# Kernel optimization log

Hardware: AMD Instinct MI355X
Metric: run time of the kernel (lower is better)

The kernel has to match this reference:

```python
import jax, jax.numpy as jnp
import numpy as np

N = 20000      # nodes
E = 100000     # edges
B = 128        # graphs in batch
F_IN = 14      # node feature dim
DIM = 64       # hidden dim
E_FEAT = 4     # edge feature dim
MLP_H = 128    # edge MLP hidden


def setup_inputs() -> dict:
    key = jax.random.key(0)
    ks = jax.random.split(key, 26)

    def rn(k, shape, fan_in):
        return jax.random.normal(k, shape, jnp.float32) / np.sqrt(fan_in)

    d = {}
    d['x'] = jax.random.normal(ks[0], (N, F_IN), jnp.float32)
    d['edge_attr'] = jax.random.uniform(ks[1], (E, E_FEAT), jnp.float32)
    d['edge_index'] = jax.random.randint(ks[2], (2, E), 0, N)
    d['batch'] = jnp.sort(jax.random.randint(ks[3], (N,), 0, B))
    # lin0
    d['lin0_w'] = rn(ks[4], (F_IN, DIM), F_IN)
    d['lin0_b'] = jnp.zeros((DIM,), jnp.float32)
    # edge MLP: Linear(4,128) -> ReLU -> Linear(128, dim*dim)
    d['mlp_w1'] = rn(ks[5], (E_FEAT, MLP_H), E_FEAT)
    d['mlp_b1'] = jnp.zeros((MLP_H,), jnp.float32)
    d['mlp_w2'] = rn(ks[6], (MLP_H, DIM * DIM), MLP_H) * 0.1
    d['mlp_b2'] = jnp.zeros((DIM * DIM,), jnp.float32)
    # NNConv root weight + bias
    d['conv_root'] = rn(ks[7], (DIM, DIM), DIM)
    d['conv_bias'] = jnp.zeros((DIM,), jnp.float32)
    # GRU (input dim DIM, hidden DIM), torch gate order r,z,n
    d['gru_wi'] = rn(ks[8], (DIM, 3 * DIM), DIM)
    d['gru_wh'] = rn(ks[9], (DIM, 3 * DIM), DIM)
    d['gru_bi'] = jnp.zeros((3 * DIM,), jnp.float32)
    d['gru_bh'] = jnp.zeros((3 * DIM,), jnp.float32)
    # Set2Set LSTM (input 2*DIM, hidden DIM), torch gate order i,f,g,o
    d['lstm_wi'] = rn(ks[10], (2 * DIM, 4 * DIM), 2 * DIM)
    d['lstm_wh'] = rn(ks[11], (DIM, 4 * DIM), DIM)
    d['lstm_bi'] = jnp.zeros((4 * DIM,), jnp.float32)
    d['lstm_bh'] = jnp.zeros((4 * DIM,), jnp.float32)
    # output head
    d['lin1_w'] = rn(ks[12], (2 * DIM, DIM), 2 * DIM)
    d['lin1_b'] = jnp.zeros((DIM,), jnp.float32)
    d['lin2_w'] = rn(ks[13], (DIM, 1), DIM)
    d['lin2_b'] = jnp.zeros((1,), jnp.float32)
    return d


def _forward(x, edge_attr, edge_index, batch,
             lin0_w, lin0_b, mlp_w1, mlp_b1, mlp_w2, mlp_b2,
             conv_root, conv_bias,
             gru_wi, gru_wh, gru_bi, gru_bh,
             lstm_wi, lstm_wh, lstm_bi, lstm_bh,
             lin1_w, lin1_b, lin2_w, lin2_b):
    src, dst = edge_index[0], edge_index[1]

    out = jax.nn.relu(x @ lin0_w + lin0_b)            # [N, DIM]
    h = out                                            # GRU hidden

    # per-edge weight matrices from edge MLP (shared across the 3 steps)
    ew = jax.nn.relu(edge_attr @ mlp_w1 + mlp_b1) @ mlp_w2 + mlp_b2
    ew = ew.reshape(E, DIM, DIM)                       # [E, DIM, DIM]
    # incoming-edge counts for scatter-mean
    cnt = jax.ops.segment_sum(jnp.ones((E,), jnp.float32), dst, num_segments=N)
    cnt = jnp.maximum(cnt, 1.0)[:, None]

    for _ in range(3):
        msg = jnp.einsum('ei,eio->eo', out[src], ew)   # gather + per-edge matmul
        agg = jax.ops.segment_sum(msg, dst, num_segments=N) / cnt
        m = jax.nn.relu(agg + out @ conv_root + conv_bias)
        # GRU cell (torch gate order: r, z, n)
        gi = m @ gru_wi + gru_bi
        gh = h @ gru_wh + gru_bh
        r = jax.nn.sigmoid(gi[:, :DIM] + gh[:, :DIM])
        z = jax.nn.sigmoid(gi[:, DIM:2 * DIM] + gh[:, DIM:2 * DIM])
        n = jnp.tanh(gi[:, 2 * DIM:] + r * gh[:, 2 * DIM:])
        h = (1.0 - z) * n + z * h
        out = h

    # Set2Set pooling, 3 processing steps
    q_star = jnp.zeros((B, 2 * DIM), jnp.float32)
    hl = jnp.zeros((B, DIM), jnp.float32)
    cl = jnp.zeros((B, DIM), jnp.float32)
    for _ in range(3):
        gates = q_star @ lstm_wi + hl @ lstm_wh + lstm_bi + lstm_bh  # [B, 4*DIM]
        i = jax.nn.sigmoid(gates[:, :DIM])
        f = jax.nn.sigmoid(gates[:, DIM:2 * DIM])
        g = jnp.tanh(gates[:, 2 * DIM:3 * DIM])
        o = jax.nn.sigmoid(gates[:, 3 * DIM:])
        cl = f * cl + i * g
        hl = o * jnp.tanh(cl)
        q = hl                                         # [B, DIM]
        e = jnp.sum(out * q[batch], axis=-1)           # [N]
        emax = jax.ops.segment_max(e, batch, num_segments=B)
        emax = jnp.where(jnp.isfinite(emax), emax, 0.0)
        a = jnp.exp(e - emax[batch])
        asum = jax.ops.segment_sum(a, batch, num_segments=B)
        a = a / jnp.maximum(asum, 1e-16)[batch]
        r_vec = jax.ops.segment_sum(a[:, None] * out, batch, num_segments=B)
        q_star = jnp.concatenate([q, r_vec], axis=-1)  # [B, 2*DIM]

    y = jax.nn.relu(q_star @ lin1_w + lin1_b) @ lin2_w + lin2_b
    return y.reshape(-1)                               # [B]


def reference(x, edge_attr, edge_index, batch,
              lin0_w, lin0_b, mlp_w1, mlp_b1, mlp_w2, mlp_b2,
              conv_root, conv_bias,
              gru_wi, gru_wh, gru_bi, gru_bh,
              lstm_wi, lstm_wh, lstm_bi, lstm_bh,
              lin1_w, lin1_b, lin2_w, lin2_b):
    return _forward(x, edge_attr, edge_index, batch,
                    lin0_w, lin0_b, mlp_w1, mlp_b1, mlp_w2, mlp_b2,
                    conv_root, conv_bias,
                    gru_wi, gru_wh, gru_bi, gru_bh,
                    lstm_wi, lstm_wh, lstm_bi, lstm_bh,
                    lin1_w, lin1_b, lin2_w, lin2_b)
```

## Files before the change

kernel.cpp:

```cpp
#include <hip/hip_runtime.h>
#include <math.h>

#define N_ 20000
#define E_ 100000
#define B_ 128
#define F_IN_ 14
#define DIM_ 64
#define E_FEAT_ 4
#define MLP_H_ 128
#define EWC_ 4096
#define PC_ 8192
#define PC2_ 8256

#define LIN0_BLKS 5000
#define DEG_BLKS 391
#define PREPB_BLKS 2064

typedef __attribute__((ext_vector_type(4))) float f32x4;
typedef __attribute__((ext_vector_type(8))) _Float16 halfx8;

__global__ __launch_bounds__(256) void setup_a(
        const float* __restrict__ x, const float* __restrict__ lw,
        const float* __restrict__ lb, float* __restrict__ out,
        const int* __restrict__ src, const int* __restrict__ dst,
        float* __restrict__ cnt, int* __restrict__ cnt_src,
        const int* __restrict__ batch, int* __restrict__ off_b,
        const float* __restrict__ w2, const float* __restrict__ b2,
        _Float16* __restrict__ Bf) {
    int b = blockIdx.x;
    int t = threadIdx.x;
    if (b < LIN0_BLKS) {
        int idx = b * 256 + t;
        int n = idx >> 6, d = idx & 63;
        float acc = lb[d];
#pragma unroll
        for (int f = 0; f < F_IN_; ++f) acc = fmaf(x[n * F_IN_ + f], lw[f * DIM_ + d], acc);
        out[idx] = acc > 0.f ? acc : 0.f;
    } else if (b < LIN0_BLKS + DEG_BLKS) {
        int e = (b - LIN0_BLKS) * 256 + t;
        if (e < E_) {
            atomicAdd(&cnt[dst[e]], 1.0f);
            atomicAdd(&cnt_src[src[e]], 1);
        }
        if (b == LIN0_BLKS && t <= B_) {
            int bb = t;
            int lo = 0, hi = N_;
            while (lo < hi) {
                int mid = (lo + hi) >> 1;
                if (batch[mid] < bb) lo = mid + 1; else hi = mid;
            }
            off_b[bb] = lo;
        }
    } else {
        int idx = (b - LIN0_BLKS - DEG_BLKS) * 256 + t;
        if (idx >= PC2_ * 64) return;
        int c16 = idx >> 10;
        int r   = idx & 1023;
        int ks  = r >> 9;
        int q   = (r >> 7) & 3;
        int lr  = (r >> 3) & 15;
        int j   = r & 7;
        int c = c16 * 16 + lr;
        int i = ks * 32 + q * 8 + j;
        float v;
        if (c < PC_) {
            int o = c >> 7, k = c & 127;
            v = w2[(size_t)k * EWC_ + i * 64 + o];
        } else {
            int o = c - PC_;
            v = b2[i * 64 + o];
        }
        Bf[idx] = (_Float16)v;
    }
}

__global__ void scan_src(const int* __restrict__ cnt_src, int* __restrict__ src_off) {
    __shared__ int part[256];
    __shared__ int off[257];
    int t = threadIdx.x;
    const int per = (N_ + 255) / 256;
    int base = t * per;
    int s = 0;
    for (int i = 0; i < per; ++i) { int b = base + i; if (b < N_) s += cnt_src[b]; }
    part[t] = s;
    __syncthreads();
    if (t == 0) {
        int a = 0;
        for (int i = 0; i < 256; ++i) { off[i] = a; a += part[i]; }
        off[256] = a;
    }
    __syncthreads();
    int run = off[t];
    for (int i = 0; i < per; ++i) {
        int b = base + i;
        if (b < N_) { src_off[b] = run; run += cnt_src[b]; }
    }
    if (t == 0) src_off[N_] = off[256];
}

__global__ __launch_bounds__(256) void scatter_mlp1(
        const int* __restrict__ src, const int* __restrict__ dst,
        int* __restrict__ cur, const int* __restrict__ src_off,
        const float* __restrict__ ea, const float* __restrict__ w1,
        const float* __restrict__ b1, int* __restrict__ dsts,
        _Float16* __restrict__ h1s) {
    __shared__ float w1s[E_FEAT_ * MLP_H_];
    __shared__ float b1s[MLP_H_];
    int t = threadIdx.x;
    if (t < MLP_H_) b1s[t] = b1[t];
    for (int i = t; i < E_FEAT_ * MLP_H_; i += 256) w1s[i] = w1[i];
    __syncthreads();
    int e = blockIdx.x * 256 + t;
    if (e >= E_) return;
    int s = src[e];
    int p = src_off[s] + atomicAdd(&cur[s], 1);
    dsts[p] = dst[e];
    float a0 = ea[e * 4 + 0], a1 = ea[e * 4 + 1];
    float a2 = ea[e * 4 + 2], a3 = ea[e * 4 + 3];
    _Float16* hrow = h1s + (size_t)p * 128;
#pragma unroll
    for (int k8 = 0; k8 < 16; ++k8) {
        halfx8 v;
#pragma unroll
        for (int j = 0; j < 8; ++j) {
            int k = k8 * 8 + j;
            float acc = b1s[k];
            acc = fmaf(a0, w1s[k], acc);
            acc = fmaf(a1, w1s[128 + k], acc);
            acc = fmaf(a2, w1s[256 + k], acc);
            acc = fmaf(a3, w1s[384 + k], acc);
            v[j] = (_Float16)(acc > 0.f ? acc : 0.f);
        }
        *(halfx8*)&hrow[k8 * 8] = v;
    }
}

__global__ __launch_bounds__(512, 4) void fused_msg(
        const float* __restrict__ out, const _Float16* __restrict__ Bf,
        const _Float16* __restrict__ h1s,
        const int* __restrict__ dsts, const int* __restrict__ src_off,
        float* __restrict__ agg) {
    __shared__ _Float16 Plds[16 * 2048];
    const int tid = threadIdx.x;
    const int lane = tid & 63;
    const int w = __builtin_amdgcn_readfirstlane(tid >> 6);
    const int lrow = lane & 15, quad = lane >> 4;
    const int nb0 = blockIdx.x * 16;

    halfx8 aG[2];
    {
        const float* orow = out + (size_t)(nb0 + lrow) * 64 + quad * 8;
#pragma unroll
        for (int ks = 0; ks < 2; ++ks) {
            float4 v0 = *(const float4*)(orow + ks * 32);
            float4 v1 = *(const float4*)(orow + ks * 32 + 4);
            aG[ks][0] = (_Float16)v0.x; aG[ks][1] = (_Float16)v0.y;
            aG[ks][2] = (_Float16)v0.z; aG[ks][3] = (_Float16)v0.w;
            aG[ks][4] = (_Float16)v1.x; aG[ks][5] = (_Float16)v1.y;
            aG[ks][6] = (_Float16)v1.z; aG[ks][7] = (_Float16)v1.w;
        }
    }

    f32x4 qf[4];
#pragma unroll
    for (int f = 0; f < 4; ++f) {
        const _Float16* bc = &Bf[(size_t)(512 + f) * 1024 + quad * 128 + lrow * 8];
        halfx8 bq0 = *(const halfx8*)bc;
        halfx8 bq1 = *(const halfx8*)(bc + 512);
        f32x4 z = (f32x4){0.f, 0.f, 0.f, 0.f};
        z = __builtin_amdgcn_mfma_f32_16x16x32_f16(aG[0], bq0, z, 0, 0, 0);
        z = __builtin_amdgcn_mfma_f32_16x16x32_f16(aG[1], bq1, z, 0, 0, 0);
        qf[f] = z;
    }

    const int n0g = nb0 + 2 * w;
    const int beg0 = src_off[n0g];
    const int end0 = src_off[n0g + 1];
    const int end1 = src_off[n0g + 2];

#pragma unroll
    for (int p = 0; p < 4; ++p) {
        if (p) __syncthreads();

#pragma unroll 8
        for (int nf = 0; nf < 16; ++nf) {
            int cl = w * 256 + nf * 16 + lrow;
            size_t tb = (size_t)(p * 128 + w * 16 + nf) * 1024 + quad * 128 + lrow * 8;
            halfx8 b0 = *(const halfx8*)&Bf[tb];
            halfx8 b1 = *(const halfx8*)&Bf[tb + 512];
            f32x4 acc = (f32x4){0.f, 0.f, 0.f, 0.f};
            acc = __builtin_amdgcn_mfma_f32_16x16x32_f16(aG[0], b0, acc, 0, 0, 0);
            acc = __builtin_amdgcn_mfma_f32_16x16x32_f16(aG[1], b1, acc, 0, 0, 0);
            int o = cl >> 7, k = cl & 127;
            int kz = k ^ (quad << 5) ^ ((o & 7) << 3);
            int base = o * 2048 + kz;
#pragma unroll
            for (int rr = 0; rr < 4; ++rr)
                Plds[base + (quad * 4 + rr) * 128] = (_Float16)acc[rr];
        }
        __syncthreads();

        int o0 = p * 16;
#pragma unroll
        for (int nn = 0; nn < 2; ++nn) {
            int nl = 2 * w + nn;
            int beg = nn ? end0 : beg0;
            int endv = nn ? end1 : end0;
            if (beg == endv) continue;
            int srcl = ((nl >> 2) << 4) | lrow;
            int rsel = nl & 3;
            float qel = rsel == 0 ? qf[p][0] : rsel == 1 ? qf[p][1]
                      : rsel == 2 ? qf[p][2] : qf[p][3];
            float qv = __shfl(qel, srcl, 64);
            halfx8 bf[4];
#pragma unroll
            for (int ks = 0; ks < 4; ++ks) {
                int kk = (ks * 32 + quad * 8) ^ ((nl >> 2) << 5) ^ ((lrow & 7) << 3);
                bf[ks] = *(const halfx8*)&Plds[lrow * 2048 + nl * 128 + kk];
            }
            for (int g = beg; g < endv; g += 16) {
                int gcnt = endv - g; if (gcnt > 16) gcnt = 16;
                int ei = lrow < gcnt ? lrow : gcnt - 1;
                int gi = g + ei;
                int dv = dsts[gi];
                halfx8 af[4];
#pragma unroll
                for (int ks = 0; ks < 4; ++ks)
                    af[ks] = *(const halfx8*)&h1s[(size_t)gi * 128 + ks * 32 + quad * 8];
                f32x4 acc = (f32x4){0.f, 0.f, 0.f, 0.f};
#pragma unroll
                for (int ks = 0; ks < 4; ++ks)
                    acc = __builtin_amdgcn_mfma_f32_16x16x32_f16(
                        af[ks], bf[ks], acc, 0, 0, 0);
#pragma unroll
                for (int rr = 0; rr < 4; ++rr) {
                    int j = quad * 4 + rr;
                    int d = __shfl(dv, j, 64);
                    if (j < gcnt) {
                        atomicAdd(&agg[(size_t)d * 64 + o0 + lrow], acc[rr] + qv);
                    }
                }
            }
        }
    }
}

__global__ __launch_bounds__(256) void gru_kernel(float* __restrict__ out,
                                                  float* __restrict__ agg,
                                                  const float* __restrict__ cnt,
                                                  const float* __restrict__ root,
                                                  const float* __restrict__ cbias,
                                                  const float* __restrict__ wi,
                                                  const float* __restrict__ wh,
                                                  const float* __restrict__ bi,
                                                  const float* __restrict__ bh) {
    __shared__ float root_s[64 * 64];
    __shared__ float h_s[64 * 64];
    __shared__ float m_s[64 * 64];
    int tid = threadIdx.x;
    int lane = tid & 63;
    int wv = __builtin_amdgcn_readfirstlane(tid >> 6);
    int nb = blockIdx.x * 64;
#pragma unroll
    for (int it = 0; it < 4; ++it) {
        int i = it * 1024 + tid * 4;
        *(float4*)&root_s[i] = *(const float4*)&root[i];
    }
#pragma unroll
    for (int it = 0; it < 4; ++it) {
        int i = it * 1024 + tid * 4;
        int gidx = nb * 64 + i;
        float4 v = gidx < N_ * 64 ? *(const float4*)&out[gidx]
                                  : (float4){0.f, 0.f, 0.f, 0.f};
        *(float4*)&h_s[i] = v;
    }
    __syncthreads();

    int nbase = nb + wv * 16;
    float a[16];
#pragma unroll
    for (int j = 0; j < 16; ++j) {
        int n = nbase + j;
        if (n < N_) {
            float c = cnt[n]; c = c > 1.f ? c : 1.f;
            a[j] = agg[(size_t)n * 64 + lane] / c + cbias[lane];
            agg[(size_t)n * 64 + lane] = 0.f;
        } else {
            a[j] = 0.f;
        }
    }
    for (int i = 0; i < 64; ++i) {
        float rv = root_s[i * 64 + lane];
#pragma unroll
        for (int j = 0; j < 16; ++j)
            a[j] = fmaf(h_s[(wv * 16 + j) * 64 + i], rv, a[j]);
    }
#pragma unroll
    for (int j = 0; j < 16; ++j)
        m_s[(wv * 16 + j) * 64 + lane] = a[j] > 0.f ? a[j] : 0.f;
    __syncthreads();

    float gr[16], gz[16], gn[16];
    {
        float b0 = bi[lane], b1 = bi[64 + lane], b2v = bi[128 + lane];
#pragma unroll
        for (int j = 0; j < 16; ++j) { gr[j] = b0; gz[j] = b1; gn[j] = b2v; }
    }
    for (int i = 0; i < 64; ++i) {
        float w0 = wi[i * 192 + lane];
        float w1 = wi[i * 192 + 64 + lane];
        float w2v = wi[i * 192 + 128 + lane];
#pragma unroll
        for (int j = 0; j < 16; ++j) {
            float mi = m_s[(wv * 16 + j) * 64 + i];
            gr[j] = fmaf(mi, w0, gr[j]);
            gz[j] = fmaf(mi, w1, gz[j]);
            gn[j] = fmaf(mi, w2v, gn[j]);
        }
    }
    float hr[16], hz[16], hn[16];
    {
        float b0 = bh[lane], b1 = bh[64 + lane], b2v = bh[128 + lane];
#pragma unroll
        for (int j = 0; j < 16; ++j) { hr[j] = b0; hz[j] = b1; hn[j] = b2v; }
    }
    for (int i = 0; i < 64; ++i) {
        float u0 = wh[i * 192 + lane];
        float u1 = wh[i * 192 + 64 + lane];
        float u2 = wh[i * 192 + 128 + lane];
#pragma unroll
        for (int j = 0; j < 16; ++j) {
            float hi = h_s[(wv * 16 + j) * 64 + i];
            hr[j] = fmaf(hi, u0, hr[j]);
            hz[j] = fmaf(hi, u1, hz[j]);
            hn[j] = fmaf(hi, u2, hn[j]);
        }
    }
#pragma unroll
    for (int j = 0; j < 16; ++j) {
        int n = nbase + j;
        if (n < N_) {
            float rg = 1.f / (1.f + expf(-(gr[j] + hr[j])));
            float zg = 1.f / (1.f + expf(-(gz[j] + hz[j])));
            float ng = tanhf(gn[j] + rg * hn[j]);
            float h = h_s[(wv * 16 + j) * 64 + lane];
            out[(size_t)n * 64 + lane] = (1.f - zg) * ng + zg * h;
        }
    }
}

__global__ __launch_bounds__(256) void lstm_all_kernel(
        const float* __restrict__ out, const int* __restrict__ off_b,
        float* __restrict__ e_ws,
        const float* __restrict__ wi, const float* __restrict__ wh,
        const float* __restrict__ bi, const float* __restrict__ bh,
        const float* __restrict__ hw1, const float* __restrict__ hb1,
        const float* __restrict__ hw2, const float* __restrict__ hb2,
        float* __restrict__ y) {
    int b = blockIdx.x;
    int t = threadIdx.x;
    __shared__ float qs[128], hs[64], cs[64], g[256];
    __shared__ float q[64];
    __shared__ float red[256], racc[256], sasum[4];

    if (t < 128) qs[t] = 0.f;
    if (t < 64) { hs[t] = 0.f; cs[t] = 0.f; }
    __syncthreads();

    int start = off_b[b], end = off_b[b + 1];

    for (int s = 0; s < 3; ++s) {
        {
            float acc = bi[t] + bh[t];
#pragma unroll 8
            for (int i = 0; i < 128; ++i) acc = fmaf(qs[i], wi[i * 256 + t], acc);
#pragma unroll 8
            for (int i = 0; i < 64; ++i) acc = fmaf(hs[i], wh[i * 256 + t], acc);
            g[t] = acc;
        }
        __syncthreads();
        if (t < 64) {
            float ig = 1.f / (1.f + expf(-g[t]));
            float fg = 1.f / (1.f + expf(-g[64 + t]));
            float gg = tanhf(g[128 + t]);
            float og = 1.f / (1.f + expf(-g[192 + t]));
            float c = fg * cs[t] + ig * gg;
            cs[t] = c;
            float h = og * tanhf(c);
            hs[t] = h;
            q[t] = h;
        }
        __syncthreads();

        float lmax = -1e30f;
        for (int n = start + t; n < end; n += 256) {
            float acc = 0.f;
#pragma unroll 16
            for (int d2 = 0; d2 < 64; ++d2) acc = fmaf(out[n * 64 + d2], q[d2], acc);
            e_ws[n] = acc;
            lmax = fmaxf(lmax, acc);
        }
        red[t] = lmax;
        __syncthreads();
        for (int s2 = 128; s2 > 0; s2 >>= 1) {
            if (t < s2) red[t] = fmaxf(red[t], red[t + s2]);
            __syncthreads();
        }
        float emax = red[0];
        int w = t >> 6, d = t & 63;
        float rl = 0.f, lasum = 0.f;
        for (int n = start + w; n < end; n += 4) {
            float a = expf(e_ws[n] - emax);
            rl = fmaf(a, out[n * 64 + d], rl);
            if (d == 0) lasum += a;
        }
        racc[t] = rl;
        if (d == 0) sasum[w] = lasum;
        __syncthreads();
        if (t < 64) {
            float r = racc[t] + racc[64 + t] + racc[128 + t] + racc[192 + t];
            float as = sasum[0] + sasum[1] + sasum[2] + sasum[3];
            as = fmaxf(as, 1e-16f);
            qs[t] = q[t];
            qs[64 + t] = r / as;
        }
        __syncthreads();
    }

    if (t < 64) {
        float acc = hb1[t];
#pragma unroll 8
        for (int i = 0; i < 128; ++i) acc = fmaf(qs[i], hw1[i * 64 + t], acc);
        acc = acc > 0.f ? acc : 0.f;
        float p = acc * hw2[t];
        for (int off = 32; off > 0; off >>= 1) p += __shfl_down(p, off, 64);
        if (t == 0) y[b] = p + hb2[0];
    }
}

extern "C" void kernel_launch(void* const* d_in, const int* in_sizes, int n_in,
                              void* d_out, int out_size, void* d_ws, size_t ws_size,
                              hipStream_t stream) {
    (void)in_sizes; (void)n_in; (void)out_size; (void)ws_size;
    const float* x        = (const float*)d_in[0];
    const float* ea       = (const float*)d_in[1];
    const int*   eidx     = (const int*)d_in[2];
    const int*   batch    = (const int*)d_in[3];
    const float* lin0_w   = (const float*)d_in[4];
    const float* lin0_b   = (const float*)d_in[5];
    const float* mlp_w1   = (const float*)d_in[6];
    const float* mlp_b1   = (const float*)d_in[7];
    const float* mlp_w2   = (const float*)d_in[8];
    const float* mlp_b2   = (const float*)d_in[9];
    const float* conv_root= (const float*)d_in[10];
    const float* conv_bias= (const float*)d_in[11];
    const float* gru_wi   = (const float*)d_in[12];
    const float* gru_wh   = (const float*)d_in[13];
    const float* gru_bi   = (const float*)d_in[14];
    const float* gru_bh   = (const float*)d_in[15];
    const float* lstm_wi  = (const float*)d_in[16];
    const float* lstm_wh  = (const float*)d_in[17];
    const float* lstm_bi  = (const float*)d_in[18];
    const float* lstm_bh  = (const float*)d_in[19];
    const float* lin1_w   = (const float*)d_in[20];
    const float* lin1_b   = (const float*)d_in[21];
    const float* lin2_w   = (const float*)d_in[22];
    const float* lin2_b   = (const float*)d_in[23];
    float* y = (float*)d_out;

    const int* src = eidx;
    const int* dst = eidx + E_;

    char* w = (char*)d_ws;
    auto carve = [&](size_t bytes) {
        char* p = w;
        w += (bytes + 255) & ~(size_t)255;
        return p;
    };
    float* out_buf = (float*)carve((size_t)N_ * DIM_ * 4);
    float* e_ws    = (float*)carve((size_t)N_ * 4);
    int*   off_b   = (int*)carve((size_t)(B_ + 1) * 4);
    _Float16* h1s  = (_Float16*)carve((size_t)E_ * MLP_H_ * 2);
    _Float16* Bf   = (_Float16*)carve((size_t)PC2_ * 64 * 2);
    int*   src_off = (int*)carve((size_t)(N_ + 1) * 4);
    int*   dsts    = (int*)carve((size_t)E_ * 4);
    char*  zero0   = w;
    float* agg     = (float*)carve((size_t)N_ * DIM_ * 4);
    float* cnt     = (float*)carve((size_t)N_ * 4);
    int*   cnt_src = (int*)carve((size_t)N_ * 4);
    int*   cur     = (int*)carve((size_t)N_ * 4);
    size_t zbytes  = (size_t)(w - zero0);

    hipMemsetAsync(zero0, 0, zbytes, stream);

    setup_a<<<LIN0_BLKS + DEG_BLKS + PREPB_BLKS, 256, 0, stream>>>(
        x, lin0_w, lin0_b, out_buf, src, dst, cnt, cnt_src, batch, off_b,
        mlp_w2, mlp_b2, Bf);
    scan_src<<<1, 256, 0, stream>>>(cnt_src, src_off);
    scatter_mlp1<<<(E_ + 255) / 256, 256, 0, stream>>>(src, dst, cur, src_off,
                                                       ea, mlp_w1, mlp_b1,
                                                       dsts, h1s);

    for (int step = 0; step < 3; ++step) {
        fused_msg<<<N_ / 16, 512, 0, stream>>>(out_buf, Bf, h1s, dsts,
                                               src_off, agg);
        gru_kernel<<<(N_ + 63) / 64, 256, 0, stream>>>(out_buf, agg, cnt,
                                                       conv_root, conv_bias,
                                                       gru_wi, gru_wh,
                                                       gru_bi, gru_bh);
    }

    lstm_all_kernel<<<B_, 256, 0, stream>>>(out_buf, off_b, e_ws,
                                            lstm_wi, lstm_wh, lstm_bi, lstm_bh,
                                            lin1_w, lin1_b, lin2_w, lin2_b, y);
}
```

Before: 614.3 us.

## Fuse message, GRU and Set2Set stages into one persistent kernel with grid barriers

Replaces the seven separate launches (three fused_msg/gru_kernel pairs plus the LSTM readout) with one persistent kernel of 512 blocks. Blocks grid-stride over node tiles and meet at atomic-counter barriers between stages, which removes launch gaps and tail effects between stages. The GRU stage now works on 32-node tiles and computes its input and hidden gate products in a single loop. The readout uses 512 threads per graph. The barrier depends on all 512 blocks being resident at once, which is assumed rather than guaranteed, and the smaller grid may expose less parallelism in the message stage.

Measured after the change: 2.007 ms. 3.27x slower.

```diff
diff --git a/kernel.cpp b/kernel.cpp
--- a/kernel.cpp
+++ b/kernel.cpp
@@ -15,6 +15,8 @@
 #define LIN0_BLKS 5000
 #define DEG_BLKS 391
 #define PREPB_BLKS 2064
+
+#define NBLK_ 512
 
 typedef __attribute__((ext_vector_type(4))) float f32x4;
 typedef __attribute__((ext_vector_type(8))) _Float16 halfx8;
@@ -135,306 +137,308 @@
     }
 }
 
-__global__ __launch_bounds__(512, 4) void fused_msg(
-        const float* __restrict__ out, const _Float16* __restrict__ Bf,
-        const _Float16* __restrict__ h1s,
-        const int* __restrict__ dsts, const int* __restrict__ src_off,
-        float* __restrict__ agg) {
-    __shared__ _Float16 Plds[16 * 2048];
+__device__ inline void gsync(int* cnt, int target) {
+    __syncthreads();
+    if (threadIdx.x == 0) {
+        __threadfence();
+        __hip_atomic_fetch_add(cnt, 1, __ATOMIC_ACQ_REL, __HIP_MEMORY_SCOPE_AGENT);
+        while (__hip_atomic_load(cnt, __ATOMIC_ACQUIRE, __HIP_MEMORY_SCOPE_AGENT) < target) {
+            __builtin_amdgcn_s_sleep(1);
+        }
+    }
+    __syncthreads();
+}
+
+__global__ __launch_bounds__(512, 4) void mega(
+        float* __restrict__ out, const _Float16* __restrict__ Bf,
+        const _Float16* __restrict__ h1s, const int* __restrict__ dsts,
+        const int* __restrict__ src_off, float* __restrict__ agg,
+        const float* __restrict__ cntf, const float* __restrict__ root,
+        const float* __restrict__ cbias, const float* __restrict__ gwi,
+        const float* __restrict__ gwh, const float* __restrict__ gbi,
+        const float* __restrict__ gbh, const int* __restrict__ off_b,
+        float* __restrict__ e_ws, const float* __restrict__ lwi,
+        const float* __restrict__ lwh, const float* __restrict__ lbi,
+        const float* __restrict__ lbh, const float* __restrict__ hw1,
+        const float* __restrict__ hb1, const float* __restrict__ hw2,
+        const float* __restrict__ hb2, float* __restrict__ y,
+        int* __restrict__ gcnt) {
+    __shared__ float smem_f[16384];
+    _Float16* Plds = (_Float16*)smem_f;
     const int tid = threadIdx.x;
     const int lane = tid & 63;
-    const int w = __builtin_amdgcn_readfirstlane(tid >> 6);
+    const int wv8 = __builtin_amdgcn_readfirstlane(tid >> 6);
     const int lrow = lane & 15, quad = lane >> 4;
-    const int nb0 = blockIdx.x * 16;
-
-    halfx8 aG[2];
-    {
-        const float* orow = out + (size_t)(nb0 + lrow) * 64 + quad * 8;
-#pragma unroll
-        for (int ks = 0; ks < 2; ++ks) {
-            float4 v0 = *(const float4*)(orow + ks * 32);
-            float4 v1 = *(const float4*)(orow + ks * 32 + 4);
-            aG[ks][0] = (_Float16)v0.x; aG[ks][1] = (_Float16)v0.y;
-            aG[ks][2] = (_Float16)v0.z; aG[ks][3] = (_Float16)v0.w;
-            aG[ks][4] = (_Float16)v1.x; aG[ks][5] = (_Float16)v1.y;
-            aG[ks][6] = (_Float16)v1.z; aG[ks][7] = (_Float16)v1.w;
-        }
-    }
-
-    f32x4 qf[4];
-#pragma unroll
-    for (int f = 0; f < 4; ++f) {
-        const _Float16* bc = &Bf[(size_t)(512 + f) * 1024 + quad * 128 + lrow * 8];
-        halfx8 bq0 = *(const halfx8*)bc;
-        halfx8 bq1 = *(const halfx8*)(bc + 512);
-        f32x4 z = (f32x4){0.f, 0.f, 0.f, 0.f};
-        z = __builtin_amdgcn_mfma_f32_16x16x32_f16(aG[0], bq0, z, 0, 0, 0);
-        z = __builtin_amdgcn_mfma_f32_16x16x32_f16(aG[1], bq1, z, 0, 0, 0);
-        qf[f] = z;
-    }
-
-    const int n0g = nb0 + 2 * w;
-    const int beg0 = src_off[n0g];
-    const int end0 = src_off[n0g + 1];
-    const int end1 = src_off[n0g + 2];
-
-#pragma unroll
-    for (int p = 0; p < 4; ++p) {
-        if (p) __syncthreads();
+    int syncno = 0;
+
+    for (int step = 0; step < 3; ++step) {
+        for (int vb = blockIdx.x; vb < N_ / 16; vb += NBLK_) {
+            __syncthreads();
+            const int nb0 = vb * 16;
+
+            halfx8 aG[2];
+            {
+                const float* orow = out + (size_t)(nb0 + lrow) * 64 + quad * 8;
+#pragma unroll
+                for (int ks = 0; ks < 2; ++ks) {
+                    float4 v0 = *(const float4*)(orow + ks * 32);
+                    float4 v1 = *(const float4*)(orow + ks * 32 + 4);
+                    aG[ks][0] = (_Float16)v0.x; aG[ks][1] = (_Float16)v0.y;
+                    aG[ks][2] = (_Float16)v0.z; aG[ks][3] = (_Float16)v0.w;
+                    aG[ks][4] = (_Float16)v1.x; aG[ks][5] = (_Float16)v1.y;
+                    aG[ks][6] = (_Float16)v1.z; aG[ks][7] = (_Float16)v1.w;
+                }
+            }
+
+            f32x4 qf[4];
+#pragma unroll
+            for (int f = 0; f < 4; ++f) {
+                const _Float16* bc = &Bf[(size_t)(512 + f) * 1024 + quad * 128 + lrow * 8];
+                halfx8 bq0 = *(const halfx8*)bc;
+                halfx8 bq1 = *(const halfx8*)(bc + 512);
+                f32x4 z = (f32x4){0.f, 0.f, 0.f, 0.f};
+                z = __builtin_amdgcn_mfma_f32_16x16x32_f16(aG[0], bq0, z, 0, 0, 0);
+                z = __builtin_amdgcn_mfma_f32_16x16x32_f16(aG[1], bq1, z, 0, 0, 0);
+                qf[f] = z;
+            }
+
+            const int n0g = nb0 + 2 * wv8;
+            const int beg0 = src_off[n0g];
+            const int end0 = src_off[n0g + 1];
+            const int end1 = src_off[n0g + 2];
+
+#pragma unroll
+            for (int p = 0; p < 4; ++p) {
+                if (p) __syncthreads();
 
 #pragma unroll 8
-        for (int nf = 0; nf < 16; ++nf) {
-            int cl = w * 256 + nf * 16 + lrow;
-            size_t tb = (size_t)(p * 128 + w * 16 + nf) * 1024 + quad * 128 + lrow * 8;
-            halfx8 b0 = *(const halfx8*)&Bf[tb];
-            halfx8 b1 = *(const halfx8*)&Bf[tb + 512];
-            f32x4 acc = (f32x4){0.f, 0.f, 0.f, 0.f};
-            acc = __builtin_amdgcn_mfma_f32_16x16x32_f16(aG[0], b0, acc, 0, 0, 0);
-            acc = __builtin_amdgcn_mfma_f32_16x16x32_f16(aG[1], b1, acc, 0, 0, 0);
-            int o = cl >> 7, k = cl & 127;
-            int kz = k ^ (quad << 5) ^ ((o & 7) << 3);
-            int base = o * 2048 + kz;
-#pragma unroll
-            for (int rr = 0; rr < 4; ++rr)
-                Plds[base + (quad * 4 + rr) * 128] = (_Float16)acc[rr];
-        }
-        __syncthreads();
-
-        int o0 = p * 16;
-#pragma unroll
-        for (int nn = 0; nn < 2; ++nn) {
-            int nl = 2 * w + nn;
-            int beg = nn ? end0 : beg0;
-            int endv = nn ? end1 : end0;
-            if (beg == endv) continue;
-            int srcl = ((nl >> 2) << 4) | lrow;
-            int rsel = nl & 3;
-            float qel = rsel == 0 ? qf[p][0] : rsel == 1 ? qf[p][1]
-                      : rsel == 2 ? qf[p][2] : qf[p][3];
-            float qv = __shfl(qel, srcl, 64);
-            halfx8 bf[4];
-#pragma unroll
-            for (int ks = 0; ks < 4; ++ks) {
-                int kk = (ks * 32 + quad * 8) ^ ((nl >> 2) << 5) ^ ((lrow & 7) << 3);
-                bf[ks] = *(const halfx8*)&Plds[lrow * 2048 + nl * 128 + kk];
-            }
-            for (int g = beg; g < endv; g += 16) {
-                int gcnt = endv - g; if (gcnt > 16) gcnt = 16;
-                int ei = lrow < gcnt ? lrow : gcnt - 1;
-                int gi = g + ei;
-                int dv = dsts[gi];
-                halfx8 af[4];
-#pragma unroll
-                for (int ks = 0; ks < 4; ++ks)
-                    af[ks] = *(const halfx8*)&h1s[(size_t)gi * 128 + ks * 32 + quad * 8];
-                f32x4 acc = (f32x4){0.f, 0.f, 0.f, 0.f};
-#pragma unroll
-                for (int ks = 0; ks < 4; ++ks)
-                    acc = __builtin_amdgcn_mfma_f32_16x16x32_f16(
-                        af[ks], bf[ks], acc, 0, 0, 0);
-#pragma unroll
-                for (int rr = 0; rr < 4; ++rr) {
-                    int j = quad * 4 + rr;
-                    int d = __shfl(dv, j, 64);
-                    if (j < gcnt) {
-                        atomicAdd(&agg[(size_t)d * 64 + o0 + lrow], acc[rr] + qv);
+                for (int nf = 0; nf < 16; ++nf) {
+                    int cl = wv8 * 256 + nf * 16 + lrow;
+                    size_t tb = (size_t)(p * 128 + wv8 * 16 + nf) * 1024 + quad * 128 + lrow * 8;
+                    halfx8 b0 = *(const halfx8*)&Bf[tb];
+                    halfx8 b1 = *(const halfx8*)&Bf[tb + 512];
+                    f32x4 acc = (f32x4){0.f, 0.f, 0.f, 0.f};
+                    acc = __builtin_amdgcn_mfma_f32_16x16x32_f16(aG[0], b0, acc, 0, 0, 0);
+                    acc = __builtin_amdgcn_mfma_f32_16x16x32_f16(aG[1], b1, acc, 0, 0, 0);
+                    int o = cl >> 7, k = cl & 127;
+                    int kz = k ^ (quad << 5) ^ ((o & 7) << 3);
+                    int base = o * 2048 + kz;
+#pragma unroll
+                    for (int rr = 0; rr < 4; ++rr)
+                        Plds[base + (quad * 4 + rr) * 128] = (_Float16)acc[rr];
+                }
+                __syncthreads();
+
+                int o0 = p * 16;
+#pragma unroll
+                for (int nn = 0; nn < 2; ++nn) {
+                    int nl = 2 * wv8 + nn;
+                    int beg = nn ? end0 : beg0;
+                    int endv = nn ? end1 : end0;
+                    if (beg == endv) continue;
+                    int srcl = ((nl >> 2) << 4) | lrow;
+                    int rsel = nl & 3;
+                    float qel = rsel == 0 ? qf[p][0] : rsel == 1 ? qf[p][1]
+                              : rsel == 2 ? qf[p][2] : qf[p][3];
+                    float qv = __shfl(qel, srcl, 64);
+                    halfx8 bf[4];
+#pragma unroll
+                    for (int ks = 0; ks < 4; ++ks) {
+                        int kk = (ks * 32 + quad * 8) ^ ((nl >> 2) << 5) ^ ((lrow & 7) << 3);
+                        bf[ks] = *(const halfx8*)&Plds[lrow * 2048 + nl * 128 + kk];
+                    }
+                    for (int g = beg; g < endv; g += 16) {
+                        int gcnt2 = endv - g; if (gcnt2 > 16) gcnt2 = 16;
+                        int ei = lrow < gcnt2 ? lrow : gcnt2 - 1;
+                        int gi = g + ei;
+                        int dv = dsts[gi];
+                        halfx8 af[4];
+#pragma unroll
+                        for (int ks = 0; ks < 4; ++ks)
+                            af[ks] = *(const halfx8*)&h1s[(size_t)gi * 128 + ks * 32 + quad * 8];
+                        f32x4 acc = (f32x4){0.f, 0.f, 0.f, 0.f};
+#pragma unroll
+                        for (int ks = 0; ks < 4; ++ks)
+                            acc = __builtin_amdgcn_mfma_f32_16x16x32_f16(
+                                af[ks], bf[ks], acc, 0, 0, 0);
+#pragma unroll
+                        for (int rr = 0; rr < 4; ++rr) {
+                            int j = quad * 4 + rr;
+                            int d = __shfl(dv, j, 64);
+                            if (j < gcnt2) {
+                                atomicAdd(&agg[(size_t)d * 64 + o0 + lrow], acc[rr] + qv);
+                            }
+                        }
                     }
                 }
             }
         }
-    }
-}
-
-__global__ __launch_bounds__(256) void gru_kernel(float* __restrict__ out,
-                                                  float* __restrict__ agg,
-                                                  const float* __restrict__ cnt,
-                                                  const float* __restrict__ root,
-                                                  const float* __restrict__ cbias,
-                                                  const float* __restrict__ wi,
-                                                  const float* __restrict__ wh,
-                                                  const float* __restrict__ bi,
-                                                  const float* __restrict__ bh) {
-    __shared__ float root_s[64 * 64];
-    __shared__ float h_s[64 * 64];
-    __shared__ float m_s[64 * 64];
-    int tid = threadIdx.x;
-    int lane = tid & 63;
-    int wv = __builtin_amdgcn_readfirstlane(tid >> 6);
-    int nb = blockIdx.x * 64;
-#pragma unroll
-    for (int it = 0; it < 4; ++it) {
-        int i = it * 1024 + tid * 4;
-        *(float4*)&root_s[i] = *(const float4*)&root[i];
-    }
-#pragma unroll
-    for (int it = 0; it < 4; ++it) {
-        int i = it * 1024 + tid * 4;
-        int gidx = nb * 64 + i;
-        float4 v = gidx < N_ * 64 ? *(const float4*)&out[gidx]
-                                  : (float4){0.f, 0.f, 0.f, 0.f};
-        *(float4*)&h_s[i] = v;
-    }
-    __syncthreads();
-
-    int nbase = nb + wv * 16;
-    float a[16];
-#pragma unroll
-    for (int j = 0; j < 16; ++j) {
-        int n = nbase + j;
-        if (n < N_) {
-            float c = cnt[n]; c = c > 1.f ? c : 1.f;
-            a[j] = agg[(size_t)n * 64 + lane] / c + cbias[lane];
-            agg[(size_t)n * 64 + lane] = 0.f;
-        } else {
-            a[j] = 0.f;
-        }
-    }
-    for (int i = 0; i < 64; ++i) {
-        float rv = root_s[i * 64 + lane];
-#pragma unroll
-        for (int j = 0; j < 16; ++j)
-            a[j] = fmaf(h_s[(wv * 16 + j) * 64 + i], rv, a[j]);
-    }
-#pragma unroll
-    for (int j = 0; j < 16; ++j)
-        m_s[(wv * 16 + j) * 64 + lane] = a[j] > 0.f ? a[j] : 0.f;
-    __syncthreads();
-
-    float gr[16], gz[16], gn[16];
-    {
-        float b0 = bi[lane], b1 = bi[64 + lane], b2v = bi[128 + lane];
-#pragma unroll
-        for (int j = 0; j < 16; ++j) { gr[j] = b0; gz[j] = b1; gn[j] = b2v; }
-    }
-    for (int i = 0; i < 64; ++i) {
-        float w0 = wi[i * 192 + lane];
-        float w1 = wi[i * 192 + 64 + lane];
-        float w2v = wi[i * 192 + 128 + lane];
-#pragma unroll
-        for (int j = 0; j < 16; ++j) {
-            float mi = m_s[(wv * 16 + j) * 64 + i];
-            gr[j] = fmaf(mi, w0, gr[j]);
-            gz[j] = fmaf(mi, w1, gz[j]);
-            gn[j] = fmaf(mi, w2v, gn[j]);
-        }
-    }
-    float hr[16], hz[16], hn[16];
-    {
-        float b0 = bh[lane], b1 = bh[64 + lane], b2v = bh[128 + lane];
-#pragma unroll
-        for (int j = 0; j < 16; ++j) { hr[j] = b0; hz[j] = b1; hn[j] = b2v; }
-    }
-    for (int i = 0; i < 64; ++i) {
-        float u0 = wh[i * 192 + lane];
-        float u1 = wh[i * 192 + 64 + lane];
-        float u2 = wh[i * 192 + 128 + lane];
-#pragma unroll
-        for (int j = 0; j < 16; ++j) {
-            float hi = h_s[(wv * 16 + j) * 64 + i];
-            hr[j] = fmaf(hi, u0, hr[j]);
-            hz[j] = fmaf(hi, u1, hz[j]);
-            hn[j] = fmaf(hi, u2, hn[j]);
-        }
-    }
-#pragma unroll
-    for (int j = 0; j < 16; ++j) {
-        int n = nbase + j;
-        if (n < N_) {
-            float rg = 1.f / (1.f + expf(-(gr[j] + hr[j])));
-            float zg = 1.f / (1.f + expf(-(gz[j] + hz[j])));
-            float ng = tanhf(gn[j] + rg * hn[j]);
-            float h = h_s[(wv * 16 + j) * 64 + lane];
-            out[(size_t)n * 64 + lane] = (1.f - zg) * ng + zg * h;
-        }
-    }
-}
-
-__global__ __launch_bounds__(256) void lstm_all_kernel(
-        const float* __restrict__ out, const int* __restrict__ off_b,
-        float* __restrict__ e_ws,
-        const float* __restrict__ wi, const float* __restrict__ wh,
-        const float* __restrict__ bi, const float* __restrict__ bh,
-        const float* __restrict__ hw1, const float* __restrict__ hb1,
-        const float* __restrict__ hw2, const float* __restrict__ hb2,
-        float* __restrict__ y) {
-    int b = blockIdx.x;
-    int t = threadIdx.x;
-    __shared__ float qs[128], hs[64], cs[64], g[256];
-    __shared__ float q[64];
-    __shared__ float red[256], racc[256], sasum[4];
-
-    if (t < 128) qs[t] = 0.f;
-    if (t < 64) { hs[t] = 0.f; cs[t] = 0.f; }
-    __syncthreads();
-
-    int start = off_b[b], end = off_b[b + 1];
-
-    for (int s = 0; s < 3; ++s) {
-        {
-            float acc = bi[t] + bh[t];
+        ++syncno; gsync(gcnt, syncno * NBLK_);
+
+        for (int vb = blockIdx.x; vb < N_ / 32; vb += NBLK_) {
+            __syncthreads();
+            float* root_s = smem_f;
+            float* h_s    = smem_f + 4096;
+            float* m_s    = smem_f + 6144;
+            const int nb = vb * 32;
+            const int wv = tid >> 6;
+#pragma unroll
+            for (int it = 0; it < 2; ++it) {
+                int i = it * 2048 + tid * 4;
+                *(float4*)&root_s[i] = *(const float4*)&root[i];
+            }
+            {
+                int i = tid * 4;
+                *(float4*)&h_s[i] = *(const float4*)&out[(size_t)nb * 64 + i];
+            }
+            __syncthreads();
+
+            int nbase = nb + wv * 4;
+            float a[4];
+#pragma unroll
+            for (int j = 0; j < 4; ++j) {
+                int n = nbase + j;
+                float c = cntf[n]; c = c > 1.f ? c : 1.f;
+                a[j] = agg[(size_t)n * 64 + lane] / c + cbias[lane];
+                agg[(size_t)n * 64 + lane] = 0.f;
+            }
+            for (int i = 0; i < 64; ++i) {
+                float rv = root_s[i * 64 + lane];
+#pragma unroll
+                for (int j = 0; j < 4; ++j)
+                    a[j] = fmaf(h_s[(wv * 4 + j) * 64 + i], rv, a[j]);
+            }
+#pragma unroll
+            for (int j = 0; j < 4; ++j)
+                m_s[(wv * 4 + j) * 64 + lane] = a[j] > 0.f ? a[j] : 0.f;
+            __syncthreads();
+
+            float gir[4], giz[4], gin[4], ghr[4], ghz[4], ghn[4];
+            {
+                float bi0 = gbi[lane], bi1 = gbi[64 + lane], bi2 = gbi[128 + lane];
+                float bh0 = gbh[lane], bh1 = gbh[64 + lane], bh2 = gbh[128 + lane];
+#pragma unroll
+                for (int j = 0; j < 4; ++j) {
+                    gir[j] = bi0; giz[j] = bi1; gin[j] = bi2;
+                    ghr[j] = bh0; ghz[j] = bh1; ghn[j] = bh2;
+                }
+            }
+            for (int i = 0; i < 64; ++i) {
+                float w0 = gwi[i * 192 + lane];
+                float w1 = gwi[i * 192 + 64 + lane];
+                float w2v = gwi[i * 192 + 128 + lane];
+                float u0 = gwh[i * 192 + lane];
+                float u1 = gwh[i * 192 + 64 + lane];
+                float u2 = gwh[i * 192 + 128 + lane];
+#pragma unroll
+                for (int j = 0; j < 4; ++j) {
+                    float mi = m_s[(wv * 4 + j) * 64 + i];
+                    float hi = h_s[(wv * 4 + j) * 64 + i];
+                    gir[j] = fmaf(mi, w0, gir[j]);
+                    giz[j] = fmaf(mi, w1, giz[j]);
+                    gin[j] = fmaf(mi, w2v, gin[j]);
+                    ghr[j] = fmaf(hi, u0, ghr[j]);
+                    ghz[j] = fmaf(hi, u1, ghz[j]);
+                    ghn[j] = fmaf(hi, u2, ghn[j]);
+                }
+            }
+#pragma unroll
+            for (int j = 0; j < 4; ++j) {
+                int n = nbase + j;
+                float rg = 1.f / (1.f + expf(-(gir[j] + ghr[j])));
+                float zg = 1.f / (1.f + expf(-(giz[j] + ghz[j])));
+                float ng = tanhf(gin[j] + rg * ghn[j]);
+                float h = h_s[(wv * 4 + j) * 64 + lane];
+                out[(size_t)n * 64 + lane] = (1.f - zg) * ng + zg * h;
+            }
+        }
+        ++syncno; gsync(gcnt, syncno * NBLK_);
+    }
+
+    if (blockIdx.x < B_) {
+        float* qs    = smem_f;
+        float* hs    = smem_f + 128;
+        float* cs    = smem_f + 192;
+        float* g     = smem_f + 256;
+        float* q     = smem_f + 512;
+        float* red   = smem_f + 576;
+        float* racc  = smem_f + 1088;
+        float* sasum = smem_f + 1600;
+        const int b = blockIdx.x, t = tid;
+        __syncthreads();
+        if (t < 128) qs[t] = 0.f;
+        if (t < 64) { hs[t] = 0.f; cs[t] = 0.f; }
+        __syncthreads();
+        int start = off_b[b], end = off_b[b + 1];
+
+        for (int s = 0; s < 3; ++s) {
+            if (t < 256) {
+                float acc = lbi[t] + lbh[t];
 #pragma unroll 8
-            for (int i = 0; i < 128; ++i) acc = fmaf(qs[i], wi[i * 256 + t], acc);
+                for (int i = 0; i < 128; ++i) acc = fmaf(qs[i], lwi[i * 256 + t], acc);
 #pragma unroll 8
-            for (int i = 0; i < 64; ++i) acc = fmaf(hs[i], wh[i * 256 + t], acc);
-            g[t] = acc;
-        }
-        __syncthreads();
+                for (int i = 0; i < 64; ++i) acc = fmaf(hs[i], lwh[i * 256 + t], acc);
+                g[t] = acc;
+            }
+            __syncthreads();
+            if (t < 64) {
+                float ig = 1.f / (1.f + expf(-g[t]));
+                float fg = 1.f / (1.f + expf(-g[64 + t]));
+                float gg = tanhf(g[128 + t]);
+                float og = 1.f / (1.f + expf(-g[192 + t]));
+                float c = fg * cs[t] + ig * gg;
+                cs[t] = c;
+                float h = og * tanhf(c);
+                hs[t] = h;
+                q[t] = h;
+            }
+            __syncthreads();
+
+            float lmax = -1e30f;
+            for (int n = start + t; n < end; n += 512) {
+                float acc = 0.f;
+#pragma unroll 16
+                for (int d2 = 0; d2 < 64; ++d2) acc = fmaf(out[n * 64 + d2], q[d2], acc);
+                e_ws[n] = acc;
+                lmax = fmaxf(lmax, acc);
+            }
+            red[t] = lmax;
+            __syncthreads();
+            for (int s2 = 256; s2 > 0; s2 >>= 1) {
+                if (t < s2) red[t] = fmaxf(red[t], red[t + s2]);
+                __syncthreads();
+            }
+            float emax = red[0];
+            int ww = t >> 6, d = t & 63;
+            float rl = 0.f, lasum = 0.f;
+            for (int n = start + ww; n < end; n += 8) {
+                float aa = expf(e_ws[n] - emax);
+                rl = fmaf(aa, out[n * 64 + d], rl);
+                if (d == 0) lasum += aa;
+            }
+            racc[t] = rl;
+            if (d == 0) sasum[ww] = lasum;
+            __syncthreads();
+            if (t < 64) {
+                float r = 0.f, as = 0.f;
+#pragma unroll
+                for (int k = 0; k < 8; ++k) { r += racc[t + 64 * k]; as += sasum[k]; }
+                as = fmaxf(as, 1e-16f);
+                qs[t] = q[t];
+                qs[64 + t] = r / as;
+            }
+            __syncthreads();
+        }
+
         if (t < 64) {
-            float ig = 1.f / (1.f + expf(-g[t]));
-            float fg = 1.f / (1.f + expf(-g[64 + t]));
-            float gg = tanhf(g[128 + t]);
-            float og = 1.f / (1.f + expf(-g[192 + t]));
-            float c = fg * cs[t] + ig * gg;
-            cs[t] = c;
-            float h = og * tanhf(c);
-            hs[t] = h;
-            q[t] = h;
-        }
-        __syncthreads();
-
-        float lmax = -1e30f;
-        for (int n = start + t; n < end; n += 256) {
-            float acc = 0.f;
-#pragma unroll 16
-            for (int d2 = 0; d2 < 64; ++d2) acc = fmaf(out[n * 64 + d2], q[d2], acc);
-            e_ws[n] = acc;
-            lmax = fmaxf(lmax, acc);
-        }
-        red[t] = lmax;
-        __syncthreads();
-        for (int s2 = 128; s2 > 0; s2 >>= 1) {
-            if (t < s2) red[t] = fmaxf(red[t], red[t + s2]);
-            __syncthreads();
-        }
-        float emax = red[0];
-        int w = t >> 6, d = t & 63;
-        float rl = 0.f, lasum = 0.f;
-        for (int n = start + w; n < end; n += 4) {
-            float a = expf(e_ws[n] - emax);
-            rl = fmaf(a, out[n * 64 + d], rl);
-            if (d == 0) lasum += a;
-        }
-        racc[t] = rl;
-        if (d == 0) sasum[w] = lasum;
-        __syncthreads();
-        if (t < 64) {
-            float r = racc[t] + racc[64 + t] + racc[128 + t] + racc[192 + t];
-            float as = sasum[0] + sasum[1] + sasum[2] + sasum[3];
-            as = fmaxf(as, 1e-16f);
-            qs[t] = q[t];
-            qs[64 + t] = r / as;
-        }
-        __syncthreads();
-    }
-
-    if (t < 64) {
-        float acc = hb1[t];
+            float acc = hb1[t];
 #pragma unroll 8
-        for (int i = 0; i < 128; ++i) acc = fmaf(qs[i], hw1[i * 64 + t], acc);
-        acc = acc > 0.f ? acc : 0.f;
-        float p = acc * hw2[t];
-        for (int off = 32; off > 0; off >>= 1) p += __shfl_down(p, off, 64);
-        if (t == 0) y[b] = p + hb2[0];
+            for (int i = 0; i < 128; ++i) acc = fmaf(qs[i], hw1[i * 64 + t], acc);
+            acc = acc > 0.f ? acc : 0.f;
+            float p = acc * hw2[t];
+            for (int off = 32; off > 0; off >>= 1) p += __shfl_down(p, off, 64);
+            if (t == 0) y[b] = p + hb2[0];
+        }
     }
 }
 
@@ -489,6 +493,7 @@
     float* cnt     = (float*)carve((size_t)N_ * 4);
     int*   cnt_src = (int*)carve((size_t)N_ * 4);
     int*   cur     = (int*)carve((size_t)N_ * 4);
+    int*   gcnt    = (int*)carve(256);
     size_t zbytes  = (size_t)(w - zero0);
 
     hipMemsetAsync(zero0, 0, zbytes, stream);
@@ -501,16 +506,9 @@
                                                        ea, mlp_w1, mlp_b1,
                                                        dsts, h1s);
 
-    for (int step = 0; step < 3; ++step) {
-        fused_msg<<<N_ / 16, 512, 0, stream>>>(out_buf, Bf, h1s, dsts,
-                                               src_off, agg);
-        gru_kernel<<<(N_ + 63) / 64, 256, 0, stream>>>(out_buf, agg, cnt,
-                                                       conv_root, conv_bias,
-                                                       gru_wi, gru_wh,
-                                                       gru_bi, gru_bh);
-    }
-
-    lstm_all_kernel<<<B_, 256, 0, stream>>>(out_buf, off_b, e_ws,
-                                            lstm_wi, lstm_wh, lstm_bi, lstm_bh,
-                                            lin1_w, lin1_b, lin2_w, lin2_b, y);
+    mega<<<NBLK_, 512, 0, stream>>>(out_buf, Bf, h1s, dsts, src_off, agg, cnt,
+                                    conv_root, conv_bias, gru_wi, gru_wh,
+                                    gru_bi, gru_bh, off_b, e_ws,
+                                    lstm_wi, lstm_wh, lstm_bi, lstm_bh,
+                                    lin1_w, lin1_b, lin2_w, lin2_b, y, gcnt);
 }
```
